# Performance work log

Measured on AMD Instinct MI355X. Metric: run time of the kernel, lower is better.

The kernel has to match this reference:

```python
import jax, jax.numpy as jnp
import numpy as np
from jax import lax

ALPHA = 1.5
N_ITER = 100


def entmax(z, alpha=ALPHA, n_iter=N_ITER):
    # z: [B, Sq, Sk] scores. Bisection for the entmax threshold tau.
    z = (alpha - 1.0) * z.astype(jnp.float32)
    S = z.shape[-1]
    z_max = jnp.max(z, axis=-1, keepdims=True)          # [B, Sq, 1]
    tau_min = z_max - 1.0
    tau_max = z_max - np.float32(S ** (1.0 - alpha))
    inv = 1.0 / (alpha - 1.0)                            # = 2.0 for alpha=1.5

    def body(carry, _):
        tmin, tmax, _ = carry
        tau = (tmin + tmax) * 0.5
        p = jnp.maximum(z - tau, 0.0) ** inv             # [B, Sq, Sk]
        Z = jnp.sum(p, axis=-1, keepdims=True)           # [B, Sq, 1]
        tmin = jnp.where(Z >= 1.0, tau, tmin)
        tmax = jnp.where(Z < 1.0, tau, tmax)
        return (tmin, tmax, tau), None

    init = (tau_min, tau_max, (tau_min + tau_max) * 0.5)
    (tmin, tmax, tau), _ = lax.scan(jax.checkpoint(body), init, None, length=n_iter)
    # faithful to the TF code: final output uses p, Z from the LAST iteration's tau
    p = jnp.maximum(z - tau, 0.0) ** inv
    Z = jnp.sum(p, axis=-1, keepdims=True)
    return p / Z


def setup_inputs() -> dict:
    key = jax.random.key(0)
    kq, kk, kv = jax.random.split(key, 3)
    B, S, D = 8, 2048, 128
    return {
        "query": jax.random.normal(kq, (B, S, D), dtype=jnp.float32),
        "key": jax.random.normal(kk, (B, S, D), dtype=jnp.float32),
        "value": jax.random.normal(kv, (B, S, D), dtype=jnp.float32),
    }


def reference(query, key, value):
    scores = jnp.einsum("bqd,bkd->bqk", query, key)      # QK^T, no scaling (as in source)
    weights = entmax(scores, alpha=ALPHA, n_iter=N_ITER)
    return jnp.einsum("bqk,bkd->bqd", weights, value)
```

## Files before the change

### kernel.cpp

```cpp
#include <hip/hip_runtime.h>

#define BB 8
#define SS 2048
#define DD 128
#define ROWS 16
#define NW 8
#define CTW 16

typedef short bf16x8 __attribute__((ext_vector_type(8)));
typedef float f32x4 __attribute__((ext_vector_type(4)));

template <int I> struct IC { static constexpr int value = I; };
template <int I, int N, typename F>
__device__ __forceinline__ void sfor(F&& f) {
  if constexpr (I < N) { f(IC<I>{}); sfor<I + 1, N>((F&&)f); }
}

__device__ __forceinline__ short f2bf(float x) {
  return __builtin_bit_cast(short, (__bf16)x);
}
__device__ __forceinline__ float bf2f(short u) {
  return __uint_as_float(((unsigned)(unsigned short)u) << 16);
}

__device__ __forceinline__ void stage_tile(const short* g, short* l) {
#pragma unroll
  for (int s = 0; s < 4; ++s) {
    __builtin_amdgcn_global_load_lds(
        (const __attribute__((address_space(1))) void*)(g + (s << 9)),
        (__attribute__((address_space(3))) void*)(l + (s << 9)), 16, 0, 0);
  }
}

__global__ __launch_bounds__(256)
void ksplit(const float* __restrict__ K, short* __restrict__ Khi) {
  const int lin  = blockIdx.x * 256 + threadIdx.x;
  const int b    = lin >> 15;
  const int rem  = lin & 32767;
  const int ct   = rem >> 8;
  const int s    = (rem >> 6) & 3;
  const int lane = rem & 63;
  const int quad = lane >> 4, m16 = lane & 15;
  const size_t elem = (size_t)(b * SS + ct * 16 + m16) * DD + s * 32 + quad * 8;
  const float4 v0 = *(const float4*)(K + elem);
  const float4 v1 = *(const float4*)(K + elem + 4);
  const float f[8] = {v0.x, v0.y, v0.z, v0.w, v1.x, v1.y, v1.z, v1.w};
  bf16x8 h;
#pragma unroll
  for (int e = 0; e < 8; ++e) h[e] = f2bf(f[e]);
  *(bf16x8*)(Khi + (size_t)lin * 8) = h;
}

__global__ __launch_bounds__(512) __attribute__((amdgpu_waves_per_eu(4)))
void attn(const float* __restrict__ Q, const short* __restrict__ Khi,
          const float* __restrict__ K, const float* __restrict__ V,
          float* __restrict__ Out) {
  __shared__ short kring[NW][2][2048];
  __shared__ unsigned short Qs[ROWS][136];
  __shared__ float rbuf[ROWS][64];
  __shared__ int   scol[ROWS][64];
  __shared__ float exM0[NW][ROWS];
  __shared__ float exM1[NW][ROWS];
  __shared__ int   rcnt[ROWS];
  __shared__ int   rovf[ROWS];
  __shared__ float tauB[ROWS], ZB[ROWS];

  const int tid  = threadIdx.x;
  const int lane = tid & 63;
  const int wid  = __builtin_amdgcn_readfirstlane(tid >> 6);
  const int quad = lane >> 4, m16 = lane & 15;
  const int b    = blockIdx.x & 7;
  const int qt   = blockIdx.x >> 3;

  const float* Qb = Q + (size_t)(b * SS + qt * ROWS) * DD;
  const float* Kb = K + (size_t)b * SS * DD;
  const float* Vb = V + (size_t)b * SS * DD;
  float*       Ob = Out + (size_t)(b * SS + qt * ROWS) * DD;
  const short* KHb = Khi + (size_t)b * SS * DD;

  if (tid < ROWS) { rcnt[tid] = 0; rovf[tid] = 0; }

  {
    const int row = tid >> 5, d = (tid & 31) * 4;
    const float4 v = *(const float4*)&Qb[row * DD + d];
    ushort4 h;
    h.x = (unsigned short)f2bf(0.5f * v.x);
    h.y = (unsigned short)f2bf(0.5f * v.y);
    h.z = (unsigned short)f2bf(0.5f * v.z);
    h.w = (unsigned short)f2bf(0.5f * v.w);
    *(ushort4*)&Qs[row][d] = h;
  }
  __syncthreads();

  bf16x8 qh[4];
#pragma unroll
  for (int s = 0; s < 4; ++s)
    qh[s] = *(const bf16x8*)&Qs[m16][s * 32 + quad * 8];

  short* ring0 = &kring[wid][0][0];
  short* ring1 = &kring[wid][1][0];
  const short* gw = KHb + ((size_t)(wid * CTW) << 11) + lane * 8;

  stage_tile(gw + 0 * 2048, ring0);
  stage_tile(gw + 1 * 2048, ring1);

  f32x4 acc[8];

  sfor<0, 8>([&](auto ic) {
    constexpr int i = ic.value;
    asm volatile("s_waitcnt vmcnt(4)" ::: "memory");
    const short* sbl = ((i & 1) ? ring1 : ring0) + lane * 8;
    f32x4 c = {0.f, 0.f, 0.f, 0.f};
    sfor<0, 4>([&](auto sc) {
      constexpr int s = sc.value;
      const bf16x8 bh = *(const bf16x8*)(sbl + (s << 9));
      c = __builtin_amdgcn_mfma_f32_16x16x32_bf16(qh[s], bh, c, 0, 0, 0);
    });
    acc[i] = c;
    asm volatile("s_waitcnt lgkmcnt(0)" ::: "memory");
    stage_tile(gw + (i + 2) * 2048, (i & 1) ? ring1 : ring0);
  });

  {
    float mx[4] = {-1e38f, -1e38f, -1e38f, -1e38f};
    sfor<0, 8>([&](auto ic) {
#pragma unroll
      for (int j = 0; j < 4; ++j) mx[j] = fmaxf(mx[j], acc[ic.value][j]);
    });
#pragma unroll
    for (int j = 0; j < 4; ++j)
#pragma unroll
      for (int s = 1; s <= 8; s <<= 1) mx[j] = fmaxf(mx[j], __shfl_xor(mx[j], s));
    if (m16 == 0) {
#pragma unroll
      for (int j = 0; j < 4; ++j) exM0[wid][4 * quad + j] = mx[j];
    }
  }
  __syncthreads();
  float M0[4];
#pragma unroll
  for (int j = 0; j < 4; ++j) {
    float m = -1e38f;
#pragma unroll
    for (int w = 0; w < NW; ++w) m = fmaxf(m, exM0[w][4 * quad + j]);
    M0[j] = m;
  }
  sfor<0, 8>([&](auto ic) {
    constexpr int i = ic.value;
    const int col = wid * 256 + i * 16 + m16;
#pragma unroll
    for (int j = 0; j < 4; ++j) {
      const int row = 4 * quad + j;
      if (acc[i][j] > M0[j] - 1.25f) {
        const int pos = atomicAdd(&rcnt[row], 1);
        if (pos < 64) { scol[row][pos] = col; rbuf[row][pos] = acc[i][j]; }
        else rovf[row] = 1;
      }
    }
  });

  sfor<8, 16>([&](auto ic) {
    constexpr int i = ic.value;
    if constexpr (i < 15) asm volatile("s_waitcnt vmcnt(4)" ::: "memory");
    else                  asm volatile("s_waitcnt vmcnt(0)" ::: "memory");
    const short* sbl = ((i & 1) ? ring1 : ring0) + lane * 8;
    f32x4 c = {0.f, 0.f, 0.f, 0.f};
    sfor<0, 4>([&](auto sc) {
      constexpr int s = sc.value;
      const bf16x8 bh = *(const bf16x8*)(sbl + (s << 9));
      c = __builtin_amdgcn_mfma_f32_16x16x32_bf16(qh[s], bh, c, 0, 0, 0);
    });
    acc[i - 8] = c;
    if constexpr (i + 2 < 16) {
      asm volatile("s_waitcnt lgkmcnt(0)" ::: "memory");
      stage_tile(gw + (i + 2) * 2048, (i & 1) ? ring1 : ring0);
    }
  });

  {
    float mx[4] = {-1e38f, -1e38f, -1e38f, -1e38f};
    sfor<0, 8>([&](auto ic) {
#pragma unroll
      for (int j = 0; j < 4; ++j) mx[j] = fmaxf(mx[j], acc[ic.value][j]);
    });
#pragma unroll
    for (int j = 0; j < 4; ++j)
#pragma unroll
      for (int s = 1; s <= 8; s <<= 1) mx[j] = fmaxf(mx[j], __shfl_xor(mx[j], s));
    if (m16 == 0) {
#pragma unroll
      for (int j = 0; j < 4; ++j) exM1[wid][4 * quad + j] = mx[j];
    }
  }
  __syncthreads();
  float M1[4];
#pragma unroll
  for (int j = 0; j < 4; ++j) {
    float m = -1e38f;
#pragma unroll
    for (int w = 0; w < NW; ++w) m = fmaxf(m, exM1[w][4 * quad + j]);
    M1[j] = m;
  }
  sfor<0, 8>([&](auto ic) {
    constexpr int i = ic.value;
    const int col = wid * 256 + (i + 8) * 16 + m16;
#pragma unroll
    for (int j = 0; j < 4; ++j) {
      const int row = 4 * quad + j;
      if (acc[i][j] > M1[j] - 1.25f) {
        const int pos = atomicAdd(&rcnt[row], 1);
        if (pos < 64) { scol[row][pos] = col; rbuf[row][pos] = acc[i][j]; }
        else rovf[row] = 1;
      }
    }
  });
  __syncthreads();


#pragma unroll
  for (int rr = 0; rr < 2; ++rr) {
    const int row = 2 * wid + rr;
    if (rovf[row]) continue;
    const int n = rcnt[row];
    const float2 q2 = *(const float2*)&Qb[row * DD + lane * 2];
    for (int i = 0; i < n; ++i) {
      const int c = scol[row][i];
      const float2 k2 = *(const float2*)&Kb[(size_t)c * DD + lane * 2];
      float t = fmaf(q2.x, k2.x, q2.y * k2.y);
#pragma unroll
      for (int s = 1; s <= 32; s <<= 1) t += __shfl_xor(t, s);
      if (lane == 0) rbuf[row][i] = 0.5f * t;
    }
  }

  {
    const int rr32 = lane >> 5;
    const int row  = 2 * wid + rr32;
    const int l32  = lane & 31;
    const int n = rcnt[row] < 64 ? rcnt[row] : 64;
    const float a0 = (l32 < n)      ? rbuf[row][l32]      : -1e38f;
    const float a1 = (l32 + 32 < n) ? rbuf[row][l32 + 32] : -1e38f;
    float Mr = fmaxf(a0, a1);
#pragma unroll
    for (int s = 1; s <= 16; s <<= 1) Mr = fmaxf(Mr, __shfl_xor(Mr, s));
    float tmn = Mr - 1.0f, tmx = Mr - 0.022097086912079608f;
    float tau = 0.5f * (tmn + tmx), Zr = 0.f;
    for (int it = 0; it < 100; ++it) {
      tau = 0.5f * (tmn + tmx);
      const float t0 = fmaxf(a0 - tau, 0.f);
      const float t1 = fmaxf(a1 - tau, 0.f);
      float zp = fmaf(t0, t0, t1 * t1);
#pragma unroll
      for (int s = 1; s <= 16; s <<= 1) zp += __shfl_xor(zp, s);
      Zr = zp;
      const float nmn = (zp >= 1.f) ? tau : tmn;
      const float nmx = (zp >= 1.f) ? tmx : tau;
      const bool ch = (nmn != tmn) || (nmx != tmx);
      tmn = nmn; tmx = nmx;
      if (!__any(ch)) break;
    }
    if (l32 == 0) { tauB[row] = tau; ZB[row] = Zr; }
  }

#pragma unroll
  for (int rr = 0; rr < 2; ++rr) {
    const int row = 2 * wid + rr;
    if (!rovf[row]) {
      const int n = rcnt[row];
      const float tau = tauB[row];
      const float iz  = 1.0f / ZB[row];
      float2 o = {0.f, 0.f};
      for (int i = 0; i < n; ++i) {
        const float rv = rbuf[row][i];
        const float tt = fmaxf(rv - tau, 0.f);
        const float pi = tt * tt * iz;
        const int   c  = scol[row][i];
        const float2 v2 = *(const float2*)&Vb[(size_t)c * DD + lane * 2];
        o.x = fmaf(pi, v2.x, o.x);
        o.y = fmaf(pi, v2.y, o.y);
      }
      *(float2*)&Ob[row * DD + lane * 2] = o;
    } else {
      float* zr = (float*)&kring[wid][0][0];
      for (int c0 = 0; c0 < 32; ++c0) {
        const int c = c0 * 64 + lane;
        const float* kp = &Kb[(size_t)c * DD];
        float t = 0.f;
        for (int d = 0; d < DD; d += 4) {
          const float4 qv = *(const float4*)&Qb[row * DD + d];
          const float4 kv = *(const float4*)&kp[d];
          t = fmaf(qv.x, kv.x, t); t = fmaf(qv.y, kv.y, t);
          t = fmaf(qv.z, kv.z, t); t = fmaf(qv.w, kv.w, t);
        }
        zr[c] = 0.5f * t;
      }
      float Mr = -1e38f;
      for (int c0 = 0; c0 < 32; ++c0) Mr = fmaxf(Mr, zr[c0 * 64 + lane]);
#pragma unroll
      for (int s = 1; s <= 32; s <<= 1) Mr = fmaxf(Mr, __shfl_xor(Mr, s));
      float tmn = Mr - 1.0f, tmx = Mr - 0.022097086912079608f;
      float tau = 0.5f * (tmn + tmx), Zr = 0.f;
      for (int it = 0; it < 100; ++it) {
        tau = 0.5f * (tmn + tmx);
        float zp = 0.f;
        for (int c0 = 0; c0 < 32; ++c0) {
          const float tt = fmaxf(zr[c0 * 64 + lane] - tau, 0.f);
          zp = fmaf(tt, tt, zp);
        }
#pragma unroll
        for (int s = 1; s <= 32; s <<= 1) zp += __shfl_xor(zp, s);
        Zr = zp;
        const float nmn = (zp >= 1.f) ? tau : tmn;
        const float nmx = (zp >= 1.f) ? tmx : tau;
        const bool ch = (nmn != tmn) || (nmx != tmx);
        tmn = nmn; tmx = nmx;
        if (!__any(ch)) break;
      }
      const float iz = 1.0f / Zr;
      float2 o = {0.f, 0.f};
      for (int c = 0; c < SS; ++c) {
        const float tt = fmaxf(zr[c] - tau, 0.f);
        if (tt > 0.f) {
          const float pi = tt * tt * iz;
          const float2 v2 = *(const float2*)&Vb[(size_t)c * DD + lane * 2];
          o.x = fmaf(pi, v2.x, o.x);
          o.y = fmaf(pi, v2.y, o.y);
        }
      }
      *(float2*)&Ob[row * DD + lane * 2] = o;
    }
  }
}

extern "C" void kernel_launch(void* const* d_in, const int* in_sizes, int n_in,
                              void* d_out, int out_size, void* d_ws, size_t ws_size,
                              hipStream_t stream) {
  const float* Q = (const float*)d_in[0];
  const float* K = (const float*)d_in[1];
  const float* V = (const float*)d_in[2];
  float* out = (float*)d_out;
  short* Khi = (short*)d_ws;

  hipLaunchKernelGGL(ksplit, dim3(BB * SS * DD / (256 * 8)), dim3(256), 0, stream,
                     K, Khi);
  hipLaunchKernelGGL(attn, dim3(BB * (SS / ROWS)), dim3(512), 0, stream,
                     Q, Khi, K, V, out);
}
```

Before: 142.3 us.

## Use single-pass 8-deep K ring, pack scores to bf16, split rows per half-wave

Replaces the two-phase 2-slot K tile ring with a single 64-step loop over an 8-slot ring of 512-element chunks, keeping about 7 loads in flight. Scores are packed to bf16 in registers so one max pass and one barrier cover all 16 column tiles, and the candidate threshold is widened from 1.25 to 1.35 to absorb the added rounding. The fp32 rescoring and PV phases now have each half-wave handle one row with float4 loads, so both rows are processed at once. The wider threshold admits more candidates, which risks more overflow fallbacks, and the larger register arrays may raise register pressure.

```diff
diff --git a/kernel.cpp b/kernel.cpp
--- a/kernel.cpp
+++ b/kernel.cpp
@@ -22,14 +22,25 @@
 __device__ __forceinline__ float bf2f(short u) {
   return __uint_as_float(((unsigned)(unsigned short)u) << 16);
 }
-
-__device__ __forceinline__ void stage_tile(const short* g, short* l) {
-#pragma unroll
-  for (int s = 0; s < 4; ++s) {
-    __builtin_amdgcn_global_load_lds(
-        (const __attribute__((address_space(1))) void*)(g + (s << 9)),
-        (__attribute__((address_space(3))) void*)(l + (s << 9)), 16, 0, 0);
-  }
+__device__ __forceinline__ unsigned pk2(float a, float b) {
+  return (unsigned)(unsigned short)f2bf(a) |
+         ((unsigned)(unsigned short)f2bf(b) << 16);
+}
+
+template <int N> __device__ __forceinline__ void wait_vm() {
+  if constexpr (N >= 6)      asm volatile("s_waitcnt vmcnt(6)" ::: "memory");
+  else if constexpr (N == 5) asm volatile("s_waitcnt vmcnt(5)" ::: "memory");
+  else if constexpr (N == 4) asm volatile("s_waitcnt vmcnt(4)" ::: "memory");
+  else if constexpr (N == 3) asm volatile("s_waitcnt vmcnt(3)" ::: "memory");
+  else if constexpr (N == 2) asm volatile("s_waitcnt vmcnt(2)" ::: "memory");
+  else if constexpr (N == 1) asm volatile("s_waitcnt vmcnt(1)" ::: "memory");
+  else                       asm volatile("s_waitcnt vmcnt(0)" ::: "memory");
+}
+
+__device__ __forceinline__ void stage1(const short* g, short* l) {
+  __builtin_amdgcn_global_load_lds(
+      (const __attribute__((address_space(1))) void*)g,
+      (__attribute__((address_space(3))) void*)l, 16, 0, 0);
 }
 
 __global__ __launch_bounds__(256)
@@ -55,12 +66,11 @@
 void attn(const float* __restrict__ Q, const short* __restrict__ Khi,
           const float* __restrict__ K, const float* __restrict__ V,
           float* __restrict__ Out) {
-  __shared__ short kring[NW][2][2048];
+  __shared__ short kring[NW][8][512];
   __shared__ unsigned short Qs[ROWS][136];
   __shared__ float rbuf[ROWS][64];
   __shared__ int   scol[ROWS][64];
-  __shared__ float exM0[NW][ROWS];
-  __shared__ float exM1[NW][ROWS];
+  __shared__ float exM[NW][ROWS];
   __shared__ int   rcnt[ROWS];
   __shared__ int   rovf[ROWS];
   __shared__ float tauB[ROWS], ZB[ROWS];
@@ -97,149 +107,99 @@
   for (int s = 0; s < 4; ++s)
     qh[s] = *(const bf16x8*)&Qs[m16][s * 32 + quad * 8];
 
-  short* ring0 = &kring[wid][0][0];
-  short* ring1 = &kring[wid][1][0];
+  short* ring = &kring[wid][0][0];
   const short* gw = KHb + ((size_t)(wid * CTW) << 11) + lane * 8;
 
-  stage_tile(gw + 0 * 2048, ring0);
-  stage_tile(gw + 1 * 2048, ring1);
-
-  f32x4 acc[8];
-
-  sfor<0, 8>([&](auto ic) {
-    constexpr int i = ic.value;
-    asm volatile("s_waitcnt vmcnt(4)" ::: "memory");
-    const short* sbl = ((i & 1) ? ring1 : ring0) + lane * 8;
-    f32x4 c = {0.f, 0.f, 0.f, 0.f};
-    sfor<0, 4>([&](auto sc) {
-      constexpr int s = sc.value;
-      const bf16x8 bh = *(const bf16x8*)(sbl + (s << 9));
-      c = __builtin_amdgcn_mfma_f32_16x16x32_bf16(qh[s], bh, c, 0, 0, 0);
-    });
-    acc[i] = c;
+  sfor<0, 7>([&](auto pc) {
+    constexpr int p = pc.value;
+    stage1(gw + p * 512, ring + p * 512);
+  });
+
+  unsigned zpk[CTW][2];
+  float mx[4] = {-1e38f, -1e38f, -1e38f, -1e38f};
+  f32x4 acc = {0.f, 0.f, 0.f, 0.f};
+
+  sfor<0, 64>([&](auto qc) {
+    constexpr int q = qc.value;
+    wait_vm<(63 - q < 6 ? 63 - q : 6)>();
     asm volatile("s_waitcnt lgkmcnt(0)" ::: "memory");
-    stage_tile(gw + (i + 2) * 2048, (i & 1) ? ring1 : ring0);
+    if constexpr (q + 7 < 64)
+      stage1(gw + (q + 7) * 512, ring + ((q + 7) & 7) * 512);
+    const bf16x8 bh = *(const bf16x8*)(ring + ((q & 7) << 9) + lane * 8);
+    constexpr int s = q & 3;
+    if constexpr (s == 0) acc = f32x4{0.f, 0.f, 0.f, 0.f};
+    acc = __builtin_amdgcn_mfma_f32_16x16x32_bf16(qh[s], bh, acc, 0, 0, 0);
+    if constexpr (s == 3) {
+      constexpr int ct = q >> 2;
+#pragma unroll
+      for (int j = 0; j < 4; ++j) mx[j] = fmaxf(mx[j], acc[j]);
+      zpk[ct][0] = pk2(acc[0], acc[1]);
+      zpk[ct][1] = pk2(acc[2], acc[3]);
+    }
   });
 
-  {
-    float mx[4] = {-1e38f, -1e38f, -1e38f, -1e38f};
-    sfor<0, 8>([&](auto ic) {
-#pragma unroll
-      for (int j = 0; j < 4; ++j) mx[j] = fmaxf(mx[j], acc[ic.value][j]);
-    });
-#pragma unroll
-    for (int j = 0; j < 4; ++j)
-#pragma unroll
-      for (int s = 1; s <= 8; s <<= 1) mx[j] = fmaxf(mx[j], __shfl_xor(mx[j], s));
-    if (m16 == 0) {
-#pragma unroll
-      for (int j = 0; j < 4; ++j) exM0[wid][4 * quad + j] = mx[j];
-    }
+#pragma unroll
+  for (int j = 0; j < 4; ++j)
+#pragma unroll
+    for (int s = 1; s <= 8; s <<= 1) mx[j] = fmaxf(mx[j], __shfl_xor(mx[j], s));
+  if (m16 == 0) {
+#pragma unroll
+    for (int j = 0; j < 4; ++j) exM[wid][4 * quad + j] = mx[j];
   }
   __syncthreads();
-  float M0[4];
+  float M4[4];
 #pragma unroll
   for (int j = 0; j < 4; ++j) {
     float m = -1e38f;
 #pragma unroll
-    for (int w = 0; w < NW; ++w) m = fmaxf(m, exM0[w][4 * quad + j]);
-    M0[j] = m;
-  }
-  sfor<0, 8>([&](auto ic) {
-    constexpr int i = ic.value;
-    const int col = wid * 256 + i * 16 + m16;
+    for (int w = 0; w < NW; ++w) m = fmaxf(m, exM[w][4 * quad + j]);
+    M4[j] = m;
+  }
+
+  sfor<0, CTW>([&](auto cc) {
+    constexpr int ct = cc.value;
+    const int col = wid * 256 + ct * 16 + m16;
+    float v[4];
+    v[0] = __uint_as_float(zpk[ct][0] << 16);
+    v[1] = __uint_as_float(zpk[ct][0] & 0xffff0000u);
+    v[2] = __uint_as_float(zpk[ct][1] << 16);
+    v[3] = __uint_as_float(zpk[ct][1] & 0xffff0000u);
 #pragma unroll
     for (int j = 0; j < 4; ++j) {
       const int row = 4 * quad + j;
-      if (acc[i][j] > M0[j] - 1.25f) {
+      if (v[j] > M4[j] - 1.35f) {
         const int pos = atomicAdd(&rcnt[row], 1);
-        if (pos < 64) { scol[row][pos] = col; rbuf[row][pos] = acc[i][j]; }
+        if (pos < 64) { scol[row][pos] = col; rbuf[row][pos] = v[j]; }
         else rovf[row] = 1;
       }
     }
   });
-
-  sfor<8, 16>([&](auto ic) {
-    constexpr int i = ic.value;
-    if constexpr (i < 15) asm volatile("s_waitcnt vmcnt(4)" ::: "memory");
-    else                  asm volatile("s_waitcnt vmcnt(0)" ::: "memory");
-    const short* sbl = ((i & 1) ? ring1 : ring0) + lane * 8;
-    f32x4 c = {0.f, 0.f, 0.f, 0.f};
-    sfor<0, 4>([&](auto sc) {
-      constexpr int s = sc.value;
-      const bf16x8 bh = *(const bf16x8*)(sbl + (s << 9));
-      c = __builtin_amdgcn_mfma_f32_16x16x32_bf16(qh[s], bh, c, 0, 0, 0);
-    });
-    acc[i - 8] = c;
-    if constexpr (i + 2 < 16) {
-      asm volatile("s_waitcnt lgkmcnt(0)" ::: "memory");
-      stage_tile(gw + (i + 2) * 2048, (i & 1) ? ring1 : ring0);
-    }
-  });
+  __syncthreads();
+
+  const int rr32 = lane >> 5;
+  const int row  = 2 * wid + rr32;
+  const int l32  = lane & 31;
+  const int nA = rcnt[2 * wid]     < 64 ? rcnt[2 * wid]     : 64;
+  const int nB = rcnt[2 * wid + 1] < 64 ? rcnt[2 * wid + 1] : 64;
+  const int nr  = rr32 ? nB : nA;
+  const int nmx = nA > nB ? nA : nB;
 
   {
-    float mx[4] = {-1e38f, -1e38f, -1e38f, -1e38f};
-    sfor<0, 8>([&](auto ic) {
-#pragma unroll
-      for (int j = 0; j < 4; ++j) mx[j] = fmaxf(mx[j], acc[ic.value][j]);
-    });
-#pragma unroll
-    for (int j = 0; j < 4; ++j)
-#pragma unroll
-      for (int s = 1; s <= 8; s <<= 1) mx[j] = fmaxf(mx[j], __shfl_xor(mx[j], s));
-    if (m16 == 0) {
-#pragma unroll
-      for (int j = 0; j < 4; ++j) exM1[wid][4 * quad + j] = mx[j];
-    }
-  }
-  __syncthreads();
-  float M1[4];
-#pragma unroll
-  for (int j = 0; j < 4; ++j) {
-    float m = -1e38f;
-#pragma unroll
-    for (int w = 0; w < NW; ++w) m = fmaxf(m, exM1[w][4 * quad + j]);
-    M1[j] = m;
-  }
-  sfor<0, 8>([&](auto ic) {
-    constexpr int i = ic.value;
-    const int col = wid * 256 + (i + 8) * 16 + m16;
-#pragma unroll
-    for (int j = 0; j < 4; ++j) {
-      const int row = 4 * quad + j;
-      if (acc[i][j] > M1[j] - 1.25f) {
-        const int pos = atomicAdd(&rcnt[row], 1);
-        if (pos < 64) { scol[row][pos] = col; rbuf[row][pos] = acc[i][j]; }
-        else rovf[row] = 1;
-      }
-    }
-  });
-  __syncthreads();
-
-
-#pragma unroll
-  for (int rr = 0; rr < 2; ++rr) {
-    const int row = 2 * wid + rr;
-    if (rovf[row]) continue;
-    const int n = rcnt[row];
-    const float2 q2 = *(const float2*)&Qb[row * DD + lane * 2];
-    for (int i = 0; i < n; ++i) {
-      const int c = scol[row][i];
-      const float2 k2 = *(const float2*)&Kb[(size_t)c * DD + lane * 2];
-      float t = fmaf(q2.x, k2.x, q2.y * k2.y);
-#pragma unroll
-      for (int s = 1; s <= 32; s <<= 1) t += __shfl_xor(t, s);
-      if (lane == 0) rbuf[row][i] = 0.5f * t;
+    const float4 q4 = *(const float4*)&Qb[row * DD + l32 * 4];
+    for (int i = 0; i < nmx; ++i) {
+      const bool act = i < nr;
+      const int c = act ? scol[row][i] : scol[row][0];
+      const float4 k4 = *(const float4*)&Kb[(size_t)c * DD + l32 * 4];
+      float t = q4.x * k4.x + q4.y * k4.y + q4.z * k4.z + q4.w * k4.w;
+#pragma unroll
+      for (int s = 1; s <= 16; s <<= 1) t += __shfl_xor(t, s);
+      if (act && l32 == 0) rbuf[row][i] = 0.5f * t;
     }
   }
 
   {
-    const int rr32 = lane >> 5;
-    const int row  = 2 * wid + rr32;
-    const int l32  = lane & 31;
-    const int n = rcnt[row] < 64 ? rcnt[row] : 64;
-    const float a0 = (l32 < n)      ? rbuf[row][l32]      : -1e38f;
-    const float a1 = (l32 + 32 < n) ? rbuf[row][l32 + 32] : -1e38f;
+    const float a0 = (l32 < nr)      ? rbuf[row][l32]      : -1e38f;
+    const float a1 = (l32 + 32 < nr) ? rbuf[row][l32 + 32] : -1e38f;
     float Mr = fmaxf(a0, a1);
 #pragma unroll
     for (int s = 1; s <= 16; s <<= 1) Mr = fmaxf(Mr, __shfl_xor(Mr, s));
@@ -262,73 +222,75 @@
     if (l32 == 0) { tauB[row] = tau; ZB[row] = Zr; }
   }
 
+  if (!rovf[row]) {
+    const float tau = tauB[row];
+    const float iz  = 1.0f / ZB[row];
+    float4 o = {0.f, 0.f, 0.f, 0.f};
+    for (int i = 0; i < nr; ++i) {
+      const float rv = rbuf[row][i];
+      const float tt = fmaxf(rv - tau, 0.f);
+      const float pi = tt * tt * iz;
+      const int   c  = scol[row][i];
+      const float4 v4 = *(const float4*)&Vb[(size_t)c * DD + l32 * 4];
+      o.x = fmaf(pi, v4.x, o.x);
+      o.y = fmaf(pi, v4.y, o.y);
+      o.z = fmaf(pi, v4.z, o.z);
+      o.w = fmaf(pi, v4.w, o.w);
+    }
+    *(float4*)&Ob[row * DD + l32 * 4] = o;
+  }
+
 #pragma unroll
   for (int rr = 0; rr < 2; ++rr) {
-    const int row = 2 * wid + rr;
-    if (!rovf[row]) {
-      const int n = rcnt[row];
-      const float tau = tauB[row];
-      const float iz  = 1.0f / ZB[row];
-      float2 o = {0.f, 0.f};
-      for (int i = 0; i < n; ++i) {
-        const float rv = rbuf[row][i];
-        const float tt = fmaxf(rv - tau, 0.f);
+    const int frow = 2 * wid + rr;
+    if (!rovf[frow]) continue;
+    float* zr = (float*)&kring[wid][0][0];
+    for (int c0 = 0; c0 < 32; ++c0) {
+      const int c = c0 * 64 + lane;
+      const float* kp = &Kb[(size_t)c * DD];
+      float t = 0.f;
+      for (int d = 0; d < DD; d += 4) {
+        const float4 qv = *(const float4*)&Qb[frow * DD + d];
+        const float4 kv = *(const float4*)&kp[d];
+        t = fmaf(qv.x, kv.x, t); t = fmaf(qv.y, kv.y, t);
+        t = fmaf(qv.z, kv.z, t); t = fmaf(qv.w, kv.w, t);
+      }
+      zr[c] = 0.5f * t;
+    }
+    float Mr = -1e38f;
+    for (int c0 = 0; c0 < 32; ++c0) Mr = fmaxf(Mr, zr[c0 * 64 + lane]);
+#pragma unroll
+    for (int s = 1; s <= 32; s <<= 1) Mr = fmaxf(Mr, __shfl_xor(Mr, s));
+    float tmn = Mr - 1.0f, tmx = Mr - 0.022097086912079608f;
+    float tau = 0.5f * (tmn + tmx), Zr = 0.f;
+    for (int it = 0; it < 100; ++it) {
+      tau = 0.5f * (tmn + tmx);
+      float zp = 0.f;
+      for (int c0 = 0; c0 < 32; ++c0) {
+        const float tt = fmaxf(zr[c0 * 64 + lane] - tau, 0.f);
+        zp = fmaf(tt, tt, zp);
+      }
+#pragma unroll
+      for (int s = 1; s <= 32; s <<= 1) zp += __shfl_xor(zp, s);
+      Zr = zp;
+      const float nmn = (zp >= 1.f) ? tau : tmn;
+      const float nmx = (zp >= 1.f) ? tmx : tau;
+      const bool ch = (nmn != tmn) || (nmx != tmx);
+      tmn = nmn; tmx = nmx;
+      if (!__any(ch)) break;
+    }
+    const float iz = 1.0f / Zr;
+    float2 o = {0.f, 0.f};
+    for (int c = 0; c < SS; ++c) {
+      const float tt = fmaxf(zr[c] - tau, 0.f);
+      if (tt > 0.f) {
         const float pi = tt * tt * iz;
-        const int   c  = scol[row][i];
         const float2 v2 = *(const float2*)&Vb[(size_t)c * DD + lane * 2];
         o.x = fmaf(pi, v2.x, o.x);
         o.y = fmaf(pi, v2.y, o.y);
       }
-      *(float2*)&Ob[row * DD + lane * 2] = o;
-    } else {
-      float* zr = (float*)&kring[wid][0][0];
-      for (int c0 = 0; c0 < 32; ++c0) {
-        const int c = c0 * 64 + lane;
-        const float* kp = &Kb[(size_t)c * DD];
-        float t = 0.f;
-        for (int d = 0; d < DD; d += 4) {
-          const float4 qv = *(const float4*)&Qb[row * DD + d];
-          const float4 kv = *(const float4*)&kp[d];
-          t = fmaf(qv.x, kv.x, t); t = fmaf(qv.y, kv.y, t);
-          t = fmaf(qv.z, kv.z, t); t = fmaf(qv.w, kv.w, t);
-        }
-        zr[c] = 0.5f * t;
-      }
-      float Mr = -1e38f;
-      for (int c0 = 0; c0 < 32; ++c0) Mr = fmaxf(Mr, zr[c0 * 64 + lane]);
-#pragma unroll
-      for (int s = 1; s <= 32; s <<= 1) Mr = fmaxf(Mr, __shfl_xor(Mr, s));
-      float tmn = Mr - 1.0f, tmx = Mr - 0.022097086912079608f;
-      float tau = 0.5f * (tmn + tmx), Zr = 0.f;
-      for (int it = 0; it < 100; ++it) {
-        tau = 0.5f * (tmn + tmx);
-        float zp = 0.f;
-        for (int c0 = 0; c0 < 32; ++c0) {
-          const float tt = fmaxf(zr[c0 * 64 + lane] - tau, 0.f);
-          zp = fmaf(tt, tt, zp);
-        }
-#pragma unroll
-        for (int s = 1; s <= 32; s <<= 1) zp += __shfl_xor(zp, s);
-        Zr = zp;
-        const float nmn = (zp >= 1.f) ? tau : tmn;
-        const float nmx = (zp >= 1.f) ? tmx : tau;
-        const bool ch = (nmn != tmn) || (nmx != tmx);
-        tmn = nmn; tmx = nmx;
-        if (!__any(ch)) break;
-      }
-      const float iz = 1.0f / Zr;
-      float2 o = {0.f, 0.f};
-      for (int c = 0; c < SS; ++c) {
-        const float tt = fmaxf(zr[c] - tau, 0.f);
-        if (tt > 0.f) {
-          const float pi = tt * tt * iz;
-          const float2 v2 = *(const float2*)&Vb[(size_t)c * DD + lane * 2];
-          o.x = fmaf(pi, v2.x, o.x);
-          o.y = fmaf(pi, v2.y, o.y);
-        }
-      }
-      *(float2*)&Ob[row * DD + lane * 2] = o;
-    }
+    }
+    *(float2*)&Ob[frow * DD + lane * 2] = o;
   }
 }
 
```

Result: faster. 128.0 us (-10.1%).
